# Performance work log

Measured on AMD Instinct MI355X. Metric: run time of the kernel, lower is better.

The kernel has to match this reference:

```python
import jax, jax.numpy as jnp
import numpy as np

D_MODEL = 1024
B, T = 4, 2048
NEG = -1000000000.0


def setup_inputs() -> dict:
    key = jax.random.key(0)
    kq, kk, kv = jax.random.split(key, 3)
    query = jax.random.normal(kq, (B, T, D_MODEL), dtype=jnp.float32)
    k = jax.random.normal(kk, (B, T, D_MODEL), dtype=jnp.float32)
    value = jax.random.normal(kv, (B, T, D_MODEL), dtype=jnp.float32)
    # causal mask: 1.0 where attention is disallowed (strictly upper triangular)
    mask = jnp.triu(jnp.ones((T, T), dtype=jnp.float32), k=1)
    return {"query": query, "key": k, "value": value, "mask": mask}


def reference(query, key, value, mask):
    # dk = sqrt(1/d_model); logits = QK^T / dk  (i.e. * sqrt(d_model)) -- faithful to source
    dk = jnp.sqrt(jnp.float32(1.0) / jnp.float32(D_MODEL))
    attn_logits = jnp.einsum("btc,bsc->bts", query, key) / dk
    attn_logits = attn_logits + mask * NEG  # mask broadcasts over batch
    score = jax.nn.softmax(attn_logits, axis=-1)
    attention = jnp.einsum("bts,bsc->btc", score, value)
    return attention
```

## Files before the change

### kernel.cpp

```cpp
#include <hip/hip_runtime.h>

#define BB 4
#define TT 2048
#define DD 1024
#define SCALE 32.0f
#define NTILE 136
#define L2E 1.4426950408889634f

typedef _Float16 f16;
typedef __attribute__((ext_vector_type(4))) _Float16 half4v;
typedef __attribute__((ext_vector_type(8))) _Float16 half8v;
typedef __attribute__((ext_vector_type(16))) float f32x16;

typedef const __attribute__((address_space(1))) unsigned int* gas_u32;
typedef __attribute__((address_space(3))) unsigned int* las_u32;

static __device__ inline void gload16(const void* g, void* l) {
    __builtin_amdgcn_global_load_lds((gas_u32)g, (las_u32)l, 16, 0, 0);
}

static __device__ inline half8v ld_frag(const f16* p) {
    half4v a = *(const half4v*)p;
    half4v b = *(const half4v*)(p + 4);
    half8v r;
    r[0] = a[0]; r[1] = a[1]; r[2] = a[2]; r[3] = a[3];
    r[4] = b[0]; r[5] = b[1]; r[6] = b[2]; r[7] = b[3];
    return r;
}


__global__ __launch_bounds__(256) void prep(const float* __restrict__ Q,
                                            const float* __restrict__ K,
                                            const float* __restrict__ V,
                                            f16* __restrict__ Qt,
                                            f16* __restrict__ Kt,
                                            f16* __restrict__ Vt) {
    __shared__ char plds[33024];
    int bid = blockIdx.x;
    int tid = threadIdx.x;
    if (bid < 2048) {
        char* rl = plds;
        int which = bid >> 10, b = (bid >> 8) & 3, mi = (bid >> 4) & 15, ks4 = bid & 15;
        const float* src = which ? K : Q;
        f16* dst = which ? Kt : Qt;
        float sc = which ? 1.0f : SCALE;
        int r = tid >> 1, h = tid & 1;
        const float* p = src + ((size_t)(b * TT + mi * 128 + r)) * DD + ks4 * 64 + h * 32;
#pragma unroll
        for (int j = 0; j < 4; ++j) {
            float4 x0 = *(const float4*)(p + j * 8);
            float4 x1 = *(const float4*)(p + j * 8 + 4);
            float vv[8] = {x0.x, x0.y, x0.z, x0.w, x1.x, x1.y, x1.z, x1.w};
            half8v hi, lo;
#pragma unroll
            for (int e = 0; e < 8; ++e) {
                float x = vv[e] * sc;
                f16 hh = (f16)x;
                hi[e] = hh;
                lo[e] = (f16)(x - (float)hh);
            }
            int ckl = h * 2 + (j >> 1);
            int shalf = j & 1;
            *(half8v*)(rl + ckl * 8192 + shalf * 2048 + r * 16) = hi;
            *(half8v*)(rl + ckl * 8192 + (2 + shalf) * 2048 + r * 16) = lo;
        }
        __syncthreads();
        char* gout = (char*)dst + ((size_t)((b * 16 + mi) * 64 + ks4 * 4)) * 8192 + tid * 128;
#pragma unroll
        for (int q = 0; q < 8; ++q)
            *(float4*)(gout + q * 16) = *(float4*)(rl + tid * 128 + q * 16);
    } else {
        float (*Vs)[129] = (float(*)[129])plds;
        int bid2 = bid - 2048;
        int b = bid2 >> 8, kb = (bid2 >> 3) & 31, nj = bid2 & 7;
        const float* src = V + ((size_t)(b * TT + kb * 64)) * DD + nj * 128;
#pragma unroll
        for (int it = 0; it < 8; ++it) {
            int f4 = it * 256 + tid;
            int row = f4 >> 5, c4 = f4 & 31;
            float4 x = *(const float4*)(src + (size_t)row * DD + c4 * 4);
            Vs[row][c4 * 4 + 0] = x.x;
            Vs[row][c4 * 4 + 1] = x.y;
            Vs[row][c4 * 4 + 2] = x.z;
            Vs[row][c4 * 4 + 3] = x.w;
        }
        __syncthreads();
#pragma unroll
        for (int qq = 0; qq < 4; ++qq) {
            int q = tid * 4 + qq;
            int ckl = q >> 9, s = (q >> 7) & 3, n = q & 127;
            half8v hv;
#pragma unroll
            for (int e = 0; e < 8; ++e) hv[e] = (f16)Vs[ckl * 32 + s * 8 + e][n];
            char* out = (char*)Vt + ((size_t)((b * 8 + nj) * 64 + kb * 2 + ckl)) * 8192
                        + s * 2048 + n * 16;
            *(half8v*)out = hv;
        }
    }
}

__global__ __launch_bounds__(256, 3) void k1_qk3(const f16* __restrict__ Qt,
                                                 const f16* __restrict__ Kt,
                                                 float* __restrict__ S) {
    __shared__ char lds[32768];

    int bid0 = blockIdx.x;
    int bid = (bid0 & 7) * (BB * NTILE / 8) + (bid0 >> 3);
    int b = bid / NTILE, rr0 = bid % NTILE;
    int mi = 0;
    while ((mi + 1) * (mi + 2) / 2 <= rr0) ++mi;
    int nj = rr0 - mi * (mi + 1) / 2;

    const char* Abase = (const char*)Qt + ((size_t)((b * 16 + mi) * 64)) * 8192;
    const char* Bbase = (const char*)Kt + ((size_t)((b * 16 + nj) * 64)) * 8192;
    float* Sb = S + (size_t)b * TT * TT + (size_t)(mi * 128) * TT + nj * 128;

    int tid = threadIdx.x;
    int lane = tid & 63;
    int wv = tid >> 6;
    int l31 = lane & 31, lhi = lane >> 5;
    int wrow = wv >> 1, wcol = wv & 1;

    int aoff[2], boff[2];
#pragma unroll
    for (int f = 0; f < 2; ++f) {
        int ra = wrow * 64 + f * 32 + l31;
        int rb = wcol * 64 + f * 32 + l31;
        aoff[f] = lhi * 2048 + ra * 16;
        boff[f] = lhi * 2048 + rb * 16;
    }
    int lane_go = wv * 2048 + lane * 16;
    int lane_lo = wv * 2048;

    f32x16 acc[2][2] = {};

#define K1_STAGE(CK, BUF)                                                       \
    {                                                                           \
        const char* ga = Abase + (size_t)(CK) * 8192 + lane_go;                 \
        const char* gb = Bbase + (size_t)(CK) * 8192 + lane_go;                 \
        char* la = lds + (BUF) * 16384 + lane_lo;                               \
        char* lb = la + 8192;                                                   \
        gload16(ga, la);                                                        \
        gload16(ga + 1024, la + 1024);                                          \
        gload16(gb, lb);                                                        \
        gload16(gb + 1024, lb + 1024);                                          \
    }

    K1_STAGE(0, 0);
    int cur = 0;
    for (int ck = 0; ck < 64; ++ck) {
        __syncthreads();
        if (ck + 1 < 64) K1_STAGE(ck + 1, cur ^ 1);
        const char* As = lds + cur * 16384;
        const char* Bs = As + 8192;
        half8v ah[2], al[2], bh[2], bl[2];
#pragma unroll
        for (int f = 0; f < 2; ++f) {
            ah[f] = *(const half8v*)(As + aoff[f]);
            al[f] = *(const half8v*)(As + aoff[f] + 4096);
            bh[f] = *(const half8v*)(Bs + boff[f]);
            bl[f] = *(const half8v*)(Bs + boff[f] + 4096);
        }
#pragma unroll
        for (int fm = 0; fm < 2; ++fm)
#pragma unroll
            for (int fn = 0; fn < 2; ++fn) {
                acc[fm][fn] = __builtin_amdgcn_mfma_f32_32x32x16_f16(ah[fm], bh[fn], acc[fm][fn], 0, 0, 0);
                acc[fm][fn] = __builtin_amdgcn_mfma_f32_32x32x16_f16(ah[fm], bl[fn], acc[fm][fn], 0, 0, 0);
                acc[fm][fn] = __builtin_amdgcn_mfma_f32_32x32x16_f16(al[fm], bh[fn], acc[fm][fn], 0, 0, 0);
            }
        cur ^= 1;
    }
#undef K1_STAGE
#pragma unroll
    for (int fm = 0; fm < 2; ++fm)
#pragma unroll
        for (int fn = 0; fn < 2; ++fn)
#pragma unroll
            for (int g = 0; g < 16; ++g) {
                int rr = (g & 3) + 8 * (g >> 2) + 4 * lhi;
                int row = wrow * 64 + fm * 32 + rr;
                int col = wcol * 64 + fn * 32 + l31;
                Sb[(size_t)row * TT + col] = acc[fm][fn][g];
            }
}

__global__ __launch_bounds__(256) void k1b3(const float* __restrict__ S,
                                            f16* __restrict__ Pt) {
    __shared__ float red[4];
    int rowid = blockIdx.x;
    int b = rowid >> 11, t = rowid & (TT - 1);
    const float* Sr = S + ((size_t)b * TT + t) * TT;
    int tid = threadIdx.x;
    int nv = t + 1;
    int mi = t >> 7, r = t & 127;
    int rowend = (mi + 1) << 7;
    int c = tid * 8;
    bool act = c < rowend;

    float v[8] = {0, 0, 0, 0, 0, 0, 0, 0};
    if (act) {
        float4 x0 = *(const float4*)(Sr + c);
        float4 x1 = *(const float4*)(Sr + c + 4);
        v[0] = x0.x; v[1] = x0.y; v[2] = x0.z; v[3] = x0.w;
        v[4] = x1.x; v[5] = x1.y; v[6] = x1.z; v[7] = x1.w;
    }

    float m = -3.0e38f;
    if (act) {
#pragma unroll
        for (int j = 0; j < 8; ++j)
            if (c + j < nv) m = fmaxf(m, v[j]);
    }
#pragma unroll
    for (int o = 32; o > 0; o >>= 1) m = fmaxf(m, __shfl_xor(m, o));
    if ((tid & 63) == 0) red[tid >> 6] = m;
    __syncthreads();
    m = fmaxf(fmaxf(red[0], red[1]), fmaxf(red[2], red[3]));
    __syncthreads();

    float e[8];
    float s = 0.f;
#pragma unroll
    for (int j = 0; j < 8; ++j) {
        e[j] = (act && c + j < nv) ? exp2f((v[j] - m) * L2E) : 0.0f;
        s += e[j];
    }
#pragma unroll
    for (int o = 32; o > 0; o >>= 1) s += __shfl_xor(s, o);
    if ((tid & 63) == 0) red[tid >> 6] = s;
    __syncthreads();
    s = red[0] + red[1] + red[2] + red[3];
    float inv = 1.0f / s;

    if (act) {
        half8v hv;
#pragma unroll
        for (int j = 0; j < 8; ++j) hv[j] = (f16)(e[j] * inv);
        int ck = c >> 5, sl = (c >> 3) & 3;
        char* dst = (char*)Pt + ((size_t)((b * 16 + mi) * 64 + ck)) * 8192
                    + sl * 2048 + r * 16;
        *(half8v*)dst = hv;
    }
}

__global__ __launch_bounds__(256, 2) void k2_pv8(const f16* __restrict__ Pt,
                                                 const f16* __restrict__ Vt,
                                                 float* __restrict__ O) {
    __shared__ char lds[65536];

    int bid0 = blockIdx.x;
    int bid = (bid0 & 7) * 64 + (bid0 >> 3);
    int b = bid >> 7, mi = (bid >> 3) & 15, nj = bid & 7;
    int kch = 2 * (mi + 1);

    const char* Abase = (const char*)Pt + ((size_t)((b * 16 + mi) * 64)) * 8192;
    const char* Bbase = (const char*)Vt + ((size_t)((b * 8 + nj) * 64)) * 8192;
    float* Ob = O + (size_t)b * TT * DD + (size_t)(mi * 128) * DD + nj * 128;

    int tid = threadIdx.x;
    int lane = tid & 63;
    int wv = tid >> 6;
    int l31 = lane & 31, lhi = lane >> 5;
    int wrow = wv >> 1, wcol = wv & 1;
    int lane16 = lane * 16;

    int arow[2], brow[2];
#pragma unroll
    for (int f = 0; f < 2; ++f) {
        arow[f] = (wrow * 64 + f * 32 + l31) * 16;
        brow[f] = (wcol * 64 + f * 32 + l31) * 16;
    }

    f32x16 acc[2][2] = {};

#define K2_STAGE(CK, BUF)                                                       \
    {                                                                           \
        const char* ga = Abase + (size_t)(CK) * 16384 + wv * 4096 + lane16;     \
        const char* gb = Bbase + (size_t)(CK) * 16384 + wv * 4096 + lane16;     \
        char* la = lds + (BUF) * 32768 + wv * 4096;                             \
        char* lb = la + 16384;                                                  \
        gload16(ga, la);                                                        \
        gload16(ga + 1024, la + 1024);                                          \
        gload16(ga + 2048, la + 2048);                                          \
        gload16(ga + 3072, la + 3072);                                          \
        gload16(gb, lb);                                                        \
        gload16(gb + 1024, lb + 1024);                                          \
        gload16(gb + 2048, lb + 2048);                                          \
        gload16(gb + 3072, lb + 3072);                                          \
    }

    K2_STAGE(0, 0);
    int cur = 0;
    for (int it = 0; it < kch; ++it) {
        __syncthreads();
        if (it + 1 < kch) K2_STAGE(it + 1, cur ^ 1);
        const char* As = lds + cur * 32768;
        const char* Bs = As + 16384;
#pragma unroll
        for (int j = 0; j < 4; ++j) {
            int slotbase = (j >> 1) * 8192 + ((j & 1) * 2 + lhi) * 2048;
            half8v a0 = *(const half8v*)(As + slotbase + arow[0]);
            half8v a1 = *(const half8v*)(As + slotbase + arow[1]);
            half8v b0 = *(const half8v*)(Bs + slotbase + brow[0]);
            half8v b1 = *(const half8v*)(Bs + slotbase + brow[1]);
            acc[0][0] = __builtin_amdgcn_mfma_f32_32x32x16_f16(a0, b0, acc[0][0], 0, 0, 0);
            acc[0][1] = __builtin_amdgcn_mfma_f32_32x32x16_f16(a0, b1, acc[0][1], 0, 0, 0);
            acc[1][0] = __builtin_amdgcn_mfma_f32_32x32x16_f16(a1, b0, acc[1][0], 0, 0, 0);
            acc[1][1] = __builtin_amdgcn_mfma_f32_32x32x16_f16(a1, b1, acc[1][1], 0, 0, 0);
        }
        cur ^= 1;
    }
#undef K2_STAGE
#pragma unroll
    for (int fm = 0; fm < 2; ++fm)
#pragma unroll
        for (int fn = 0; fn < 2; ++fn)
#pragma unroll
            for (int g = 0; g < 16; ++g) {
                int rr = (g & 3) + 8 * (g >> 2) + 4 * lhi;
                int row = wrow * 64 + fm * 32 + rr;
                int col = wcol * 64 + fn * 32 + l31;
                Ob[(size_t)row * DD + col] = acc[fm][fn][g];
            }
}

__global__ __launch_bounds__(256, 2) void k1_qk(const float* __restrict__ Q,
                                                const float* __restrict__ Kmat,
                                                float* __restrict__ S) {
    __shared__ f16 Ah[128][36], Al[128][36], Bh[128][36], Bl[128][36];
    int bid = blockIdx.x;
    int b = bid / NTILE, r = bid % NTILE;
    int mi = 0;
    while ((mi + 1) * (mi + 2) / 2 <= r) ++mi;
    int nj = r - mi * (mi + 1) / 2;
    const float* Qb = Q + ((size_t)b * TT + (size_t)mi * 128) * DD;
    const float* Kb = Kmat + ((size_t)b * TT + (size_t)nj * 128) * DD;
    float* Sb = S + (size_t)b * TT * TT + (size_t)(mi * 128) * TT + nj * 128;
    int tid = threadIdx.x;
    int lane = tid & 63;
    int wave = tid >> 6;
    int l31 = lane & 31, lhi = lane >> 5;
    int wrow = wave >> 1, wcol = wave & 1;
    int r0 = tid >> 1;
    int c0 = (tid & 1) * 16;
    f32x16 acc[2][2] = {};
    float4 abuf[4], bbuf[4];
#pragma unroll
    for (int j = 0; j < 4; ++j) {
        abuf[j] = *(const float4*)(Qb + (size_t)r0 * DD + c0 + 4 * j);
        bbuf[j] = *(const float4*)(Kb + (size_t)r0 * DD + c0 + 4 * j);
    }
    for (int ch = 0; ch < DD / 32; ++ch) {
        __syncthreads();
#pragma unroll
        for (int j = 0; j < 4; ++j) {
            float4 a = abuf[j], bq = bbuf[j];
            float ax[4] = {a.x * SCALE, a.y * SCALE, a.z * SCALE, a.w * SCALE};
            float bx[4] = {bq.x, bq.y, bq.z, bq.w};
            half4v ahv, alv, bhv, blv;
#pragma unroll
            for (int e = 0; e < 4; ++e) {
                f16 h = (f16)ax[e];
                ahv[e] = h;
                alv[e] = (f16)(ax[e] - (float)h);
                f16 g = (f16)bx[e];
                bhv[e] = g;
                blv[e] = (f16)(bx[e] - (float)g);
            }
            *(half4v*)&Ah[r0][c0 + 4 * j] = ahv;
            *(half4v*)&Al[r0][c0 + 4 * j] = alv;
            *(half4v*)&Bh[r0][c0 + 4 * j] = bhv;
            *(half4v*)&Bl[r0][c0 + 4 * j] = blv;
        }
        __syncthreads();
        if (ch + 1 < DD / 32) {
            int ck = (ch + 1) * 32;
#pragma unroll
            for (int j = 0; j < 4; ++j) {
                abuf[j] = *(const float4*)(Qb + (size_t)r0 * DD + ck + c0 + 4 * j);
                bbuf[j] = *(const float4*)(Kb + (size_t)r0 * DD + ck + c0 + 4 * j);
            }
        }
#pragma unroll
        for (int ks = 0; ks < 2; ++ks) {
            int kb = ks * 16 + lhi * 8;
            half8v ahf[2], alf[2], bhf[2], blf[2];
#pragma unroll
            for (int f = 0; f < 2; ++f) {
                ahf[f] = ld_frag(&Ah[wrow * 64 + f * 32 + l31][kb]);
                alf[f] = ld_frag(&Al[wrow * 64 + f * 32 + l31][kb]);
                bhf[f] = ld_frag(&Bh[wcol * 64 + f * 32 + l31][kb]);
                blf[f] = ld_frag(&Bl[wcol * 64 + f * 32 + l31][kb]);
            }
#pragma unroll
            for (int fm = 0; fm < 2; ++fm)
#pragma unroll
                for (int fn = 0; fn < 2; ++fn) {
                    acc[fm][fn] = __builtin_amdgcn_mfma_f32_32x32x16_f16(ahf[fm], bhf[fn], acc[fm][fn], 0, 0, 0);
                    acc[fm][fn] = __builtin_amdgcn_mfma_f32_32x32x16_f16(ahf[fm], blf[fn], acc[fm][fn], 0, 0, 0);
                    acc[fm][fn] = __builtin_amdgcn_mfma_f32_32x32x16_f16(alf[fm], bhf[fn], acc[fm][fn], 0, 0, 0);
                }
        }
    }
#pragma unroll
    for (int fm = 0; fm < 2; ++fm)
#pragma unroll
        for (int fn = 0; fn < 2; ++fn)
#pragma unroll
            for (int g = 0; g < 16; ++g) {
                int rr = (g & 3) + 8 * (g >> 2) + 4 * lhi;
                int row = wrow * 64 + fm * 32 + rr;
                int col = wcol * 64 + fn * 32 + l31;
                Sb[(size_t)row * TT + col] = acc[fm][fn][g];
            }
}

__global__ __launch_bounds__(256) void k1b_softmax(const float* __restrict__ S,
                                                   f16* __restrict__ P) {
    __shared__ float red[4];
    int rowid = blockIdx.x;
    int b = rowid >> 11, t = rowid & (TT - 1);
    const float* Sr = S + (size_t)b * TT * TT + (size_t)t * TT;
    f16* Pr = P + (size_t)b * TT * TT + (size_t)t * TT;
    int tid = threadIdx.x;
    int nv = t + 1;
    int rowend = ((t >> 7) + 1) << 7;
    float m = -3.0e38f;
    for (int c = tid; c < nv; c += 256) m = fmaxf(m, Sr[c]);
#pragma unroll
    for (int o = 32; o > 0; o >>= 1) m = fmaxf(m, __shfl_xor(m, o));
    if ((tid & 63) == 0) red[tid >> 6] = m;
    __syncthreads();
    m = fmaxf(fmaxf(red[0], red[1]), fmaxf(red[2], red[3]));
    __syncthreads();
    float s = 0.f;
    for (int c = tid; c < nv; c += 256) s += exp2f((Sr[c] - m) * L2E);
#pragma unroll
    for (int o = 32; o > 0; o >>= 1) s += __shfl_xor(s, o);
    if ((tid & 63) == 0) red[tid >> 6] = s;
    __syncthreads();
    s = red[0] + red[1] + red[2] + red[3];
    float inv = 1.0f / s;
    for (int c = tid; c < rowend; c += 256) {
        float p = (c < nv) ? exp2f((Sr[c] - m) * L2E) * inv : 0.0f;
        Pr[c] = (f16)p;
    }
}

__global__ __launch_bounds__(256, 2) void k2_pv(const f16* __restrict__ P,
                                                const float* __restrict__ V,
                                                float* __restrict__ O) {
    __shared__ f16 Pa[128][36];
    __shared__ f16 Vtt[128][36];
    int bid = blockIdx.x;
    int b = bid >> 7;
    int rest = bid & 127;
    int mi = rest >> 3, nj = rest & 7;
    int kend = (mi + 1) * 128;
    const f16* Pb = P + (size_t)b * TT * TT + (size_t)(mi * 128) * TT;
    const float* Vb = V + (size_t)b * TT * DD + nj * 128;
    float* Ob = O + (size_t)b * TT * DD + (size_t)(mi * 128) * DD + nj * 128;
    int tid = threadIdx.x;
    int lane = tid & 63;
    int wave = tid >> 6;
    int l31 = lane & 31, lhi = lane >> 5;
    int wrow = wave >> 1, wcol = wave & 1;
    f32x16 acc[2][2] = {};
    int pr = tid >> 1, pc = (tid & 1) * 16;
    int vk = tid >> 3, vn = (tid & 7) * 16;
    uint2 pbuf[4];
    float4 vbuf[4];
#pragma unroll
    for (int j = 0; j < 4; ++j) {
        pbuf[j] = *(const uint2*)(Pb + (size_t)pr * TT + pc + 4 * j);
        vbuf[j] = *(const float4*)(Vb + (size_t)vk * DD + vn + 4 * j);
    }
    for (int ck = 0; ck < kend; ck += 32) {
        __syncthreads();
#pragma unroll
        for (int j = 0; j < 4; ++j) {
            *(uint2*)&Pa[pr][pc + 4 * j] = pbuf[j];
            float4 v = vbuf[j];
            float vv[4] = {v.x, v.y, v.z, v.w};
            int n0 = vn + 4 * j;
#pragma unroll
            for (int e = 0; e < 4; ++e) {
                int n = n0 + e;
                Vtt[n][vk ^ ((((unsigned)n >> 4) & 3) << 3)] = (f16)vv[e];
            }
        }
        __syncthreads();
        if (ck + 32 < kend) {
            int cn = ck + 32;
#pragma unroll
            for (int j = 0; j < 4; ++j) {
                pbuf[j] = *(const uint2*)(Pb + (size_t)pr * TT + cn + pc + 4 * j);
                vbuf[j] = *(const float4*)(Vb + (size_t)(cn + vk) * DD + vn + 4 * j);
            }
        }
#pragma unroll
        for (int ks = 0; ks < 2; ++ks) {
            int kb = ks * 16 + lhi * 8;
            half8v paf[2], vbf[2];
#pragma unroll
            for (int f = 0; f < 2; ++f) {
                paf[f] = ld_frag(&Pa[wrow * 64 + f * 32 + l31][kb]);
                int n = wcol * 64 + f * 32 + l31;
                int kbs = kb ^ ((((unsigned)n >> 4) & 3) << 3);
                vbf[f] = ld_frag(&Vtt[n][kbs]);
            }
#pragma unroll
            for (int fm = 0; fm < 2; ++fm)
#pragma unroll
                for (int fn = 0; fn < 2; ++fn)
                    acc[fm][fn] = __builtin_amdgcn_mfma_f32_32x32x16_f16(paf[fm], vbf[fn], acc[fm][fn], 0, 0, 0);
        }
    }
#pragma unroll
    for (int fm = 0; fm < 2; ++fm)
#pragma unroll
        for (int fn = 0; fn < 2; ++fn)
#pragma unroll
            for (int g = 0; g < 16; ++g) {
                int rr = (g & 3) + 8 * (g >> 2) + 4 * lhi;
                int row = wrow * 64 + fm * 32 + rr;
                int col = wcol * 64 + fn * 32 + l31;
                Ob[(size_t)row * DD + col] = acc[fm][fn][g];
            }
}

__global__ __launch_bounds__(256) void fa_fallback(const float* __restrict__ Q,
                                                   const float* __restrict__ Kmat,
                                                   const float* __restrict__ V,
                                                   float* __restrict__ O) {
    __shared__ float qs[DD];
    __shared__ float osum[DD];
    __shared__ float red[4];
    int rowid = blockIdx.x;
    int b = rowid >> 11, t = rowid & (TT - 1);
    const float* q = Q + ((size_t)b * TT + t) * DD;
    int tid = threadIdx.x;
    for (int j = tid; j < DD; j += 256) { qs[j] = q[j] * SCALE; osum[j] = 0.f; }
    __syncthreads();
    float m = -3.0e38f, l = 0.f;
    for (int s = 0; s <= t; ++s) {
        const float* kr = Kmat + ((size_t)b * TT + s) * DD;
        float part = 0.f;
#pragma unroll
        for (int j = 0; j < 4; ++j) part += qs[tid * 4 + j] * kr[tid * 4 + j];
#pragma unroll
        for (int o = 32; o > 0; o >>= 1) part += __shfl_xor(part, o);
        if ((tid & 63) == 0) red[tid >> 6] = part;
        __syncthreads();
        float dot = red[0] + red[1] + red[2] + red[3];
        float mn = fmaxf(m, dot);
        float f = exp2f((m - mn) * 1.44269504f);
        float e = exp2f((dot - mn) * 1.44269504f);
        l = l * f + e;
        const float* vr = V + ((size_t)b * TT + s) * DD;
#pragma unroll
        for (int j = 0; j < 4; ++j) {
            int c = tid * 4 + j;
            osum[c] = osum[c] * f + e * vr[c];
        }
        m = mn;
        __syncthreads();
    }
    float inv = 1.f / l;
    for (int j = tid; j < DD; j += 256) O[((size_t)b * TT + t) * DD + j] = osum[j] * inv;
}

extern "C" void kernel_launch(void* const* d_in, const int* in_sizes, int n_in,
                              void* d_out, int out_size, void* d_ws, size_t ws_size,
                              hipStream_t stream) {
    const float* Q = (const float*)d_in[0];
    const float* K = (const float*)d_in[1];
    const float* V = (const float*)d_in[2];
    float* O = (float*)d_out;

    const size_t MB = 1024 * 1024;
    const size_t QT_B = 32 * MB, KT_B = 32 * MB, VT_B = 16 * MB, S_B = 64 * MB;
    const size_t FULL = QT_B + KT_B + VT_B + S_B;

    size_t sbytes = (size_t)BB * TT * TT * 4;
    size_t pbytes = (size_t)BB * TT * TT * 2;

    if (ws_size >= FULL) {
        f16* Qt = (f16*)d_ws;
        f16* Kt = (f16*)((char*)d_ws + QT_B);
        f16* Vt = (f16*)((char*)d_ws + QT_B + KT_B);
        float* S = (float*)((char*)d_ws + QT_B + KT_B + VT_B);
        f16* Pt = (f16*)d_ws;
        hipLaunchKernelGGL(prep, dim3(3072), dim3(256), 0, stream, Q, K, V, Qt, Kt, Vt);
        hipLaunchKernelGGL(k1_qk3, dim3(BB * NTILE), dim3(256), 0, stream, Qt, Kt, S);
        hipLaunchKernelGGL(k1b3, dim3(BB * TT), dim3(256), 0, stream, S, Pt);
        hipLaunchKernelGGL(k2_pv8, dim3(512), dim3(256), 0, stream, Pt, Vt, O);
    } else if (ws_size >= sbytes + pbytes) {
        float* S = (float*)d_ws;
        f16* P = (f16*)((char*)d_ws + sbytes);
        hipLaunchKernelGGL(k1_qk, dim3(BB * NTILE), dim3(256), 0, stream, Q, K, S);
        hipLaunchKernelGGL(k1b_softmax, dim3(BB * TT), dim3(256), 0, stream, S, P);
        hipLaunchKernelGGL(k2_pv, dim3(BB * 16 * 8), dim3(256), 0, stream, P, V, O);
    } else {
        hipLaunchKernelGGL(fa_fallback, dim3(BB * TT), dim3(256), 0, stream, Q, K, V, O);
    }
}
```

Measured before the change: 160.7 us.

## Fuse tile-local softmax into QK kernel and rescale P in PV kernel

Drops the separate softmax kernel and the fp32 score matrix round-trip. The QK kernel now computes per-tile row max and exp sums, writes unnormalized fp16 exponentials directly in the PV layout, and stores per-tile (max, sum) stats. The PV kernel combines the stats into per-tile rescale factors and multiplies the P fragments by them before the MFMAs. This removes 64MB of fp32 writes and reads plus a launch, at the cost of extra VALU work in the PV inner loop and scattered 2-byte stores of P. Unnormalized fp16 exponentials relative to tile max may lose precision.

```diff
diff --git a/kernel.cpp b/kernel.cpp
--- a/kernel.cpp
+++ b/kernel.cpp
@@ -99,9 +99,10 @@
     }
 }
 
-__global__ __launch_bounds__(256, 3) void k1_qk3(const f16* __restrict__ Qt,
+__global__ __launch_bounds__(256, 3) void k1_qk9(const f16* __restrict__ Qt,
                                                  const f16* __restrict__ Kt,
-                                                 float* __restrict__ S) {
+                                                 f16* __restrict__ Pt,
+                                                 float2* __restrict__ stats) {
     __shared__ char lds[32768];
 
     int bid0 = blockIdx.x;
@@ -113,7 +114,7 @@
 
     const char* Abase = (const char*)Qt + ((size_t)((b * 16 + mi) * 64)) * 8192;
     const char* Bbase = (const char*)Kt + ((size_t)((b * 16 + nj) * 64)) * 8192;
-    float* Sb = S + (size_t)b * TT * TT + (size_t)(mi * 128) * TT + nj * 128;
+    char* Ptb = (char*)Pt + ((size_t)((b * 16 + mi) * 64 + nj * 4)) * 8192;
 
     int tid = threadIdx.x;
     int lane = tid & 63;
@@ -172,82 +173,68 @@
         cur ^= 1;
     }
 #undef K1_STAGE
+
+    __syncthreads();
+    float* mpart = (float*)lds;
+    float* spart = (float*)(lds + 1024);
+    bool diag = (nj == mi);
+
 #pragma unroll
     for (int fm = 0; fm < 2; ++fm)
 #pragma unroll
-        for (int fn = 0; fn < 2; ++fn)
-#pragma unroll
-            for (int g = 0; g < 16; ++g) {
-                int rr = (g & 3) + 8 * (g >> 2) + 4 * lhi;
-                int row = wrow * 64 + fm * 32 + rr;
-                int col = wcol * 64 + fn * 32 + l31;
-                Sb[(size_t)row * TT + col] = acc[fm][fn][g];
-            }
-}
-
-__global__ __launch_bounds__(256) void k1b3(const float* __restrict__ S,
-                                            f16* __restrict__ Pt) {
-    __shared__ float red[4];
-    int rowid = blockIdx.x;
-    int b = rowid >> 11, t = rowid & (TT - 1);
-    const float* Sr = S + ((size_t)b * TT + t) * TT;
-    int tid = threadIdx.x;
-    int nv = t + 1;
-    int mi = t >> 7, r = t & 127;
-    int rowend = (mi + 1) << 7;
-    int c = tid * 8;
-    bool act = c < rowend;
-
-    float v[8] = {0, 0, 0, 0, 0, 0, 0, 0};
-    if (act) {
-        float4 x0 = *(const float4*)(Sr + c);
-        float4 x1 = *(const float4*)(Sr + c + 4);
-        v[0] = x0.x; v[1] = x0.y; v[2] = x0.z; v[3] = x0.w;
-        v[4] = x1.x; v[5] = x1.y; v[6] = x1.z; v[7] = x1.w;
-    }
-
-    float m = -3.0e38f;
-    if (act) {
-#pragma unroll
-        for (int j = 0; j < 8; ++j)
-            if (c + j < nv) m = fmaxf(m, v[j]);
-    }
-#pragma unroll
-    for (int o = 32; o > 0; o >>= 1) m = fmaxf(m, __shfl_xor(m, o));
-    if ((tid & 63) == 0) red[tid >> 6] = m;
-    __syncthreads();
-    m = fmaxf(fmaxf(red[0], red[1]), fmaxf(red[2], red[3]));
-    __syncthreads();
-
-    float e[8];
-    float s = 0.f;
-#pragma unroll
-    for (int j = 0; j < 8; ++j) {
-        e[j] = (act && c + j < nv) ? exp2f((v[j] - m) * L2E) : 0.0f;
-        s += e[j];
-    }
-#pragma unroll
-    for (int o = 32; o > 0; o >>= 1) s += __shfl_xor(s, o);
-    if ((tid & 63) == 0) red[tid >> 6] = s;
-    __syncthreads();
-    s = red[0] + red[1] + red[2] + red[3];
-    float inv = 1.0f / s;
-
-    if (act) {
-        half8v hv;
-#pragma unroll
-        for (int j = 0; j < 8; ++j) hv[j] = (f16)(e[j] * inv);
-        int ck = c >> 5, sl = (c >> 3) & 3;
-        char* dst = (char*)Pt + ((size_t)((b * 16 + mi) * 64 + ck)) * 8192
-                    + sl * 2048 + r * 16;
-        *(half8v*)dst = hv;
-    }
-}
-
-__global__ __launch_bounds__(256, 2) void k2_pv8(const f16* __restrict__ Pt,
+        for (int g = 0; g < 16; ++g) {
+            int rr = (g & 3) + 8 * (g >> 2) + 4 * lhi;
+            int lrow = wrow * 64 + fm * 32 + rr;
+            float v0 = acc[fm][0][g], v1 = acc[fm][1][g];
+            if (diag) {
+                if (wcol * 64 + l31 > lrow) v0 = -3.0e38f;
+                if (wcol * 64 + 32 + l31 > lrow) v1 = -3.0e38f;
+            }
+            float mv = fmaxf(v0, v1);
+#pragma unroll
+            for (int o = 16; o > 0; o >>= 1) mv = fmaxf(mv, __shfl_xor(mv, o));
+            if (l31 == 0) mpart[wcol * 128 + lrow] = mv;
+        }
+    __syncthreads();
+
+#pragma unroll
+    for (int fm = 0; fm < 2; ++fm)
+#pragma unroll
+        for (int g = 0; g < 16; ++g) {
+            int rr = (g & 3) + 8 * (g >> 2) + 4 * lhi;
+            int lrow = wrow * 64 + fm * 32 + rr;
+            float mt = fmaxf(mpart[lrow], mpart[128 + lrow]);
+            float sum = 0.f;
+#pragma unroll
+            for (int fn = 0; fn < 2; ++fn) {
+                float v = acc[fm][fn][g];
+                bool msk = diag && (wcol * 64 + fn * 32 + l31 > lrow);
+                float ev = msk ? 0.f : exp2f((v - mt) * L2E);
+                sum += ev;
+                int ckl = wcol * 2 + fn;
+                int s = l31 >> 3, el = l31 & 7;
+                *(f16*)(Ptb + ckl * 8192 + s * 2048 + lrow * 16 + el * 2) = (f16)ev;
+            }
+#pragma unroll
+            for (int o = 16; o > 0; o >>= 1) sum += __shfl_xor(sum, o);
+            if (l31 == 0) spart[wcol * 128 + lrow] = sum;
+        }
+    __syncthreads();
+
+    if (tid < 128) {
+        float mt = fmaxf(mpart[tid], mpart[128 + tid]);
+        float lt = spart[tid] + spart[128 + tid];
+        float2 st; st.x = mt; st.y = lt;
+        stats[((size_t)((b * 16 + mi) * 16 + nj)) * 128 + tid] = st;
+    }
+}
+
+__global__ __launch_bounds__(256, 2) void k2_pv9(const f16* __restrict__ Pt,
                                                  const f16* __restrict__ Vt,
+                                                 const float2* __restrict__ stats,
                                                  float* __restrict__ O) {
     __shared__ char lds[65536];
+    __shared__ float ftab[16][128];
 
     int bid0 = blockIdx.x;
     int bid = (bid0 & 7) * 64 + (bid0 >> 3);
@@ -291,10 +278,36 @@
     }
 
     K2_STAGE(0, 0);
+    if (kch > 1) K2_STAGE(1, 1);
+
+    int nt = mi + 1;
+    if (tid < 128) {
+        const float2* sp = stats + ((size_t)(b * 16 + mi) * 16) * 128 + tid;
+        float m = -3.0e38f;
+        for (int t = 0; t < nt; ++t) m = fmaxf(m, sp[(size_t)t * 128].x);
+        float l = 0.f;
+        for (int t = 0; t < nt; ++t) {
+            float2 s = sp[(size_t)t * 128];
+            l += s.y * exp2f((s.x - m) * L2E);
+        }
+        float invl = 1.0f / l;
+        for (int t = 0; t < nt; ++t) {
+            float2 s = sp[(size_t)t * 128];
+            ftab[t][tid] = exp2f((s.x - m) * L2E) * invl;
+        }
+    }
+    __syncthreads();
+
     int cur = 0;
     for (int it = 0; it < kch; ++it) {
         __syncthreads();
-        if (it + 1 < kch) K2_STAGE(it + 1, cur ^ 1);
+        if (it + 1 < kch) {
+            int nx = it + 1;
+            K2_STAGE(nx, cur ^ 1);
+        }
+        int t = it >> 1;
+        f16 h0 = (f16)ftab[t][wrow * 64 + l31];
+        f16 h1 = (f16)ftab[t][wrow * 64 + 32 + l31];
         const char* As = lds + cur * 32768;
         const char* Bs = As + 16384;
 #pragma unroll
@@ -302,6 +315,8 @@
             int slotbase = (j >> 1) * 8192 + ((j & 1) * 2 + lhi) * 2048;
             half8v a0 = *(const half8v*)(As + slotbase + arow[0]);
             half8v a1 = *(const half8v*)(As + slotbase + arow[1]);
+#pragma unroll
+            for (int e2 = 0; e2 < 8; ++e2) { a0[e2] *= h0; a1[e2] *= h1; }
             half8v b0 = *(const half8v*)(Bs + slotbase + brow[0]);
             half8v b1 = *(const half8v*)(Bs + slotbase + brow[1]);
             acc[0][0] = __builtin_amdgcn_mfma_f32_32x32x16_f16(a0, b0, acc[0][0], 0, 0, 0);
@@ -580,22 +595,21 @@
     float* O = (float*)d_out;
 
     const size_t MB = 1024 * 1024;
-    const size_t QT_B = 32 * MB, KT_B = 32 * MB, VT_B = 16 * MB, S_B = 64 * MB;
-    const size_t FULL = QT_B + KT_B + VT_B + S_B;
+    const size_t QT_B = 32 * MB, KT_B = 32 * MB, VT_B = 16 * MB, PT_B = 32 * MB;
+    const size_t NEED = QT_B + KT_B + VT_B + PT_B + 1 * MB;
 
     size_t sbytes = (size_t)BB * TT * TT * 4;
     size_t pbytes = (size_t)BB * TT * TT * 2;
 
-    if (ws_size >= FULL) {
+    if (ws_size >= NEED) {
         f16* Qt = (f16*)d_ws;
         f16* Kt = (f16*)((char*)d_ws + QT_B);
         f16* Vt = (f16*)((char*)d_ws + QT_B + KT_B);
-        float* S = (float*)((char*)d_ws + QT_B + KT_B + VT_B);
-        f16* Pt = (f16*)d_ws;
+        f16* Pt = (f16*)((char*)d_ws + QT_B + KT_B + VT_B);
+        float2* stats = (float2*)((char*)d_ws + QT_B + KT_B + VT_B + PT_B);
         hipLaunchKernelGGL(prep, dim3(3072), dim3(256), 0, stream, Q, K, V, Qt, Kt, Vt);
-        hipLaunchKernelGGL(k1_qk3, dim3(BB * NTILE), dim3(256), 0, stream, Qt, Kt, S);
-        hipLaunchKernelGGL(k1b3, dim3(BB * TT), dim3(256), 0, stream, S, Pt);
-        hipLaunchKernelGGL(k2_pv8, dim3(512), dim3(256), 0, stream, Pt, Vt, O);
+        hipLaunchKernelGGL(k1_qk9, dim3(BB * NTILE), dim3(256), 0, stream, Qt, Kt, Pt, stats);
+        hipLaunchKernelGGL(k2_pv9, dim3(512), dim3(256), 0, stream, Pt, Vt, stats, O);
     } else if (ws_size >= sbytes + pbytes) {
         float* S = (float*)d_ws;
         f16* P = (f16*)((char*)d_ws + sbytes);
```

Result: slower. 173.3 us (+7.8%).
